# Performance work log

Hardware: AMD Instinct MI355X
Metric: run time of the kernel (lower is better)

## Reference

```python
import jax, jax.numpy as jnp
import numpy as np

INPUT_SIZE = 256
HIDDEN_SIZE = 256


def _linear_params(key, in_dim, out_dim):
    # PyTorch nn.Linear default init: U(-1/sqrt(in_dim), 1/sqrt(in_dim))
    k1, k2 = jax.random.split(key)
    bound = 1.0 / np.sqrt(in_dim)
    W = jax.random.uniform(k1, (out_dim, in_dim), jnp.float32, -bound, bound)
    b = jax.random.uniform(k2, (out_dim,), jnp.float32, -bound, bound)
    return W, b


def setup_inputs() -> dict:
    key = jax.random.key(0)
    keys = jax.random.split(key, 7)
    B = 65536
    x = jax.random.normal(keys[0], (B, INPUT_SIZE), jnp.float32)
    h_prev = jax.random.normal(keys[1], (B, HIDDEN_SIZE), jnp.float32)
    W_ir, b_ir = _linear_params(keys[2], INPUT_SIZE, HIDDEN_SIZE)
    W_iz, b_iz = _linear_params(keys[3], INPUT_SIZE, HIDDEN_SIZE)
    W_in, b_in = _linear_params(keys[4], INPUT_SIZE, HIDDEN_SIZE)
    W_hz, b_hz = _linear_params(keys[5], HIDDEN_SIZE, HIDDEN_SIZE)
    W_hn, b_hn = _linear_params(keys[6], HIDDEN_SIZE, HIDDEN_SIZE)
    # NOTE: weights_hr exists in the torch module but is never used in forward
    # (the source uses weights_hz for the reset gate too), so it is omitted.
    return {
        'x': x, 'h_prev': h_prev,
        'W_ir': W_ir, 'b_ir': b_ir,
        'W_iz': W_iz, 'b_iz': b_iz,
        'W_in': W_in, 'b_in': b_in,
        'W_hz': W_hz, 'b_hz': b_hz,
        'W_hn': W_hn, 'b_hn': b_hn,
    }


def reference(x, h_prev, W_ir, b_ir, W_iz, b_iz, W_in, b_in, W_hz, b_hz, W_hn, b_hn):
    # Faithful to source: both z and r use the hz projection of h_prev.
    hz = h_prev @ W_hz.T + b_hz                       # [B, H]
    z = jax.nn.sigmoid(x @ W_iz.T + b_iz + hz)        # update gate
    r = jax.nn.sigmoid(x @ W_ir.T + b_ir + hz)        # reset gate (bug: uses hz)
    g = jnp.tanh(x @ W_in.T + b_in + r * (h_prev @ W_hn.T + b_hn))
    h_new = (1.0 - z) * g + z * h_prev
    return h_new
```

## Files before the change

### kernel.cpp

```cpp
#include <hip/hip_runtime.h>
#include <hip/hip_bf16.h>

typedef __bf16 bf16x8 __attribute__((ext_vector_type(8)));
typedef __bf16 bf16x4 __attribute__((ext_vector_type(4)));
typedef float  f32x4  __attribute__((ext_vector_type(4)));

#define HID   256
#define BM    64
#define PITCH 264

__global__ void __launch_bounds__(256) prepack_frag(
    const float* __restrict__ w0, const float* __restrict__ w1,
    const float* __restrict__ w2, const float* __restrict__ w3,
    const float* __restrict__ w4, __bf16* __restrict__ wb)
{
    int t    = blockIdx.x * 256 + threadIdx.x;
    int lane = t & 63;
    int cb   = (t >> 6) & 15;
    int gk   = t >> 10;
    int g    = gk % 5;
    int ks   = gk / 5;
    const float* W = g == 0 ? w0 : g == 1 ? w1 : g == 2 ? w2 : g == 3 ? w3 : w4;
    int row = cb * 16 + (lane & 15);
    int k0  = ks * 32 + (lane >> 4) * 8;
    float4 p = *(const float4*)(W + row * HID + k0);
    float4 q = *(const float4*)(W + row * HID + k0 + 4);
    bf16x8 o;
    o[0]=(__bf16)p.x; o[1]=(__bf16)p.y; o[2]=(__bf16)p.z; o[3]=(__bf16)p.w;
    o[4]=(__bf16)q.x; o[5]=(__bf16)q.y; o[6]=(__bf16)q.z; o[7]=(__bf16)q.w;
    *(bf16x8*)(wb + (size_t)t * 8) = o;
}

#define MFMA1(D, A_, B_) D = __builtin_amdgcn_mfma_f32_16x16x32_bf16(A_, B_, D, 0, 0, 0)

#define MFMA12(MF, AX, AH, B_) do {                                   \
    _Pragma("unroll")                                                 \
    for (int nf = 0; nf < 2; ++nf) {                                  \
        MFMA1(az[MF][nf],  AX, B_[2 + nf]);                           \
        MFMA1(ar[MF][nf],  AX, B_[0 + nf]);                           \
        MFMA1(anx[MF][nf], AX, B_[4 + nf]);                           \
        MFMA1(az[MF][nf],  AH, B_[6 + nf]);                           \
        MFMA1(ar[MF][nf],  AH, B_[6 + nf]);                           \
        MFMA1(anh[MF][nf], AH, B_[8 + nf]);                           \
    }                                                                 \
} while (0)

#define LOADB(DST, KK) do {                                           \
    _Pragma("unroll")                                                 \
    for (int g = 0; g < 5; ++g)                                       \
        _Pragma("unroll")                                             \
        for (int nf = 0; nf < 2; ++nf)                                \
            DST[g * 2 + nf] =                                         \
                *(const bf16x8*)(wbase + ((KK) * 5 + g) * 8192 + nf * 512); \
} while (0)

#define LOADB_SLOW(DST, KK) do {                                      \
    _Pragma("unroll")                                                 \
    for (int g = 0; g < 5; ++g)                                       \
        _Pragma("unroll")                                             \
        for (int nf = 0; nf < 2; ++nf) {                              \
            const float* pp = wsrc[g] + ((wn * 2 + nf) * 16 + lr) * HID + (KK) * 32 + lg * 8; \
            float4 c0 = *(const float4*)(pp), c1 = *(const float4*)(pp + 4); \
            bf16x8 u;                                                 \
            u[0]=(__bf16)c0.x; u[1]=(__bf16)c0.y; u[2]=(__bf16)c0.z; u[3]=(__bf16)c0.w; \
            u[4]=(__bf16)c1.x; u[5]=(__bf16)c1.y; u[6]=(__bf16)c1.z; u[7]=(__bf16)c1.w; \
            DST[g * 2 + nf] = u;                                      \
        }                                                             \
} while (0)

#define CLUSTER(B_, KC) do {                                          \
    const int kb = (KC) * 32 + lg * 8;                                \
    bf16x8 a0x = *(const bf16x8*)(xt + (0 * 16 + lr) * PITCH + kb);   \
    bf16x8 a0h = *(const bf16x8*)(ht + (0 * 16 + lr) * PITCH + kb);   \
    bf16x8 a1x = *(const bf16x8*)(xt + (1 * 16 + lr) * PITCH + kb);   \
    bf16x8 a1h = *(const bf16x8*)(ht + (1 * 16 + lr) * PITCH + kb);   \
    MFMA12(0, a0x, a0h, B_);                                          \
    a0x = *(const bf16x8*)(xt + (2 * 16 + lr) * PITCH + kb);          \
    a0h = *(const bf16x8*)(ht + (2 * 16 + lr) * PITCH + kb);          \
    MFMA12(1, a1x, a1h, B_);                                          \
    a1x = *(const bf16x8*)(xt + (3 * 16 + lr) * PITCH + kb);          \
    a1h = *(const bf16x8*)(ht + (3 * 16 + lr) * PITCH + kb);          \
    MFMA12(2, a0x, a0h, B_);                                          \
    MFMA12(3, a1x, a1h, B_);                                          \
} while (0)

template<bool PACKED>
__global__ void __launch_bounds__(512, 2) gru_fused(
    const float* __restrict__ x,  const float* __restrict__ h,
    const __bf16* __restrict__ wb,
    const float* __restrict__ w_ir, const float* __restrict__ w_iz,
    const float* __restrict__ w_in, const float* __restrict__ w_hz,
    const float* __restrict__ w_hn,
    const float* __restrict__ b_ir, const float* __restrict__ b_iz,
    const float* __restrict__ b_in, const float* __restrict__ b_hz,
    const float* __restrict__ b_hn,
    float* __restrict__ out)
{
    __shared__ __bf16 xt[BM * PITCH];
    __shared__ __bf16 ht[BM * PITCH];

    const int t    = threadIdx.x;
    const int row0 = blockIdx.x * BM;
    const int lane = t & 63;
    const int wn   = t >> 6;
    const int lr   = lane & 15;
    const int lg   = lane >> 4;

    const float* wsrc[5] = { w_ir, w_iz, w_in, w_hz, w_hn };
    const __bf16* wbase = wb + wn * 1024 + lane * 8;

    f32x4 vx[8], vh[8];
#pragma unroll
    for (int i = 0; i < 8; ++i) {
        int c = i * 512 + t, r = c >> 6, k4 = (c & 63) * 4;
        vx[i] = __builtin_nontemporal_load((const f32x4*)(x + (size_t)(row0 + r) * HID + k4));
        vh[i] = __builtin_nontemporal_load((const f32x4*)(h + (size_t)(row0 + r) * HID + k4));
    }
    bf16x8 Ba[10], Bb[10];
    if (PACKED) LOADB(Ba, wn);
#pragma unroll
    for (int i = 0; i < 8; ++i) {
        int c = i * 512 + t, r = c >> 6, k4 = (c & 63) * 4;
        bf16x4 bx, bh;
        bx[0] = (__bf16)vx[i][0]; bx[1] = (__bf16)vx[i][1]; bx[2] = (__bf16)vx[i][2]; bx[3] = (__bf16)vx[i][3];
        bh[0] = (__bf16)vh[i][0]; bh[1] = (__bf16)vh[i][1]; bh[2] = (__bf16)vh[i][2]; bh[3] = (__bf16)vh[i][3];
        *(bf16x4*)(xt + r * PITCH + k4) = bx;
        *(bf16x4*)(ht + r * PITCH + k4) = bh;
    }
    __syncthreads();

    f32x4 az[4][2], ar[4][2], anx[4][2], anh[4][2];
#pragma unroll
    for (int mf = 0; mf < 4; ++mf)
#pragma unroll
        for (int nf = 0; nf < 2; ++nf) {
            az[mf][nf] = (f32x4)0.0f; ar[mf][nf] = (f32x4)0.0f;
            anx[mf][nf] = (f32x4)0.0f; anh[mf][nf] = (f32x4)0.0f;
        }

#pragma unroll
    for (int i2 = 0; i2 < 4; ++i2) {
        const int kA = (wn + 2 * i2)     & 7;
        const int kB = (wn + 2 * i2 + 1) & 7;
        const int kN = (wn + 2 * i2 + 2) & 7;
        if (PACKED) LOADB(Bb, kB); else LOADB_SLOW(Ba, kA);
        CLUSTER(Ba, kA);
        if (PACKED) { if (i2 < 3) LOADB(Ba, kN); } else LOADB_SLOW(Bb, kB);
        CLUSTER(Bb, kB);
    }

    float bz[2], br[2], bnx[2], bnh[2];
#pragma unroll
    for (int nf = 0; nf < 2; ++nf) {
        int col = wn * 32 + nf * 16 + lr;
        bz[nf]  = b_iz[col] + b_hz[col];
        br[nf]  = b_ir[col] + b_hz[col];
        bnx[nf] = b_in[col];
        bnh[nf] = b_hn[col];
    }
#pragma unroll
    for (int mf = 0; mf < 4; ++mf)
#pragma unroll
        for (int nf = 0; nf < 2; ++nf)
#pragma unroll
            for (int i = 0; i < 4; ++i) {
                int rl  = mf * 16 + lg * 4 + i;
                int col = wn * 32 + nf * 16 + lr;
                float z  = 1.0f / (1.0f + __expf(-(az[mf][nf][i] + bz[nf])));
                float r  = 1.0f / (1.0f + __expf(-(ar[mf][nf][i] + br[nf])));
                float e2 = __expf(2.0f * (anx[mf][nf][i] + bnx[nf] + r * (anh[mf][nf][i] + bnh[nf])));
                float g  = 1.0f - 2.0f / (e2 + 1.0f);
                float hp = (float)ht[rl * PITCH + col];
                __builtin_nontemporal_store((1.0f - z) * g + z * hp,
                                            out + (size_t)(row0 + rl) * HID + col);
            }
}

extern "C" void kernel_launch(void* const* d_in, const int* in_sizes, int n_in,
                              void* d_out, int out_size, void* d_ws, size_t ws_size,
                              hipStream_t stream) {
    const float* x    = (const float*)d_in[0];
    const float* h    = (const float*)d_in[1];
    const float* w_ir = (const float*)d_in[2];
    const float* b_ir = (const float*)d_in[3];
    const float* w_iz = (const float*)d_in[4];
    const float* b_iz = (const float*)d_in[5];
    const float* w_in = (const float*)d_in[6];
    const float* b_in = (const float*)d_in[7];
    const float* w_hz = (const float*)d_in[8];
    const float* b_hz = (const float*)d_in[9];
    const float* w_hn = (const float*)d_in[10];
    const float* b_hn = (const float*)d_in[11];
    float* out = (float*)d_out;

    const int B = in_sizes[0] / HID;
    const size_t wb_bytes = (size_t)5 * HID * HID * sizeof(__bf16);

    if (ws_size >= wb_bytes) {
        __bf16* wb = (__bf16*)d_ws;
        prepack_frag<<<160, 256, 0, stream>>>(w_ir, w_iz, w_in, w_hz, w_hn, wb);
        gru_fused<true><<<B / BM, 512, 0, stream>>>(
            x, h, wb, nullptr, nullptr, nullptr, nullptr, nullptr,
            b_ir, b_iz, b_in, b_hz, b_hn, out);
    } else {
        gru_fused<false><<<B / BM, 512, 0, stream>>>(
            x, h, nullptr, w_ir, w_iz, w_in, w_hz, w_hn,
            b_ir, b_iz, b_in, b_hz, b_hn, out);
    }
}
```

Measured before the change: 97.59 us.

## Make GRU kernel persistent with double-buffered LDS prefetch of next tile

```diff
diff --git a/kernel.cpp b/kernel.cpp
--- a/kernel.cpp
+++ b/kernel.cpp
@@ -84,6 +84,39 @@
     MFMA12(3, a1x, a1h, B_);                                          \
 } while (0)
 
+#define KPAIR(I2) do {                                                \
+    const int kA = (wn + 2 * (I2))     & 7;                           \
+    const int kB = (wn + 2 * (I2) + 1) & 7;                           \
+    const int kN = (wn + 2 * (I2) + 2) & 7;                           \
+    if (PACKED) LOADB(Bb, kB); else LOADB_SLOW(Ba, kA);               \
+    CLUSTER(Ba, kA);                                                  \
+    if (PACKED) LOADB(Ba, kN); else LOADB_SLOW(Bb, kB);               \
+    CLUSTER(Bb, kB);                                                  \
+} while (0)
+
+#define PF_ISSUE(Q) do {                                              \
+    _Pragma("unroll")                                                 \
+    for (int i = 0; i < 2; ++i) {                                     \
+        int r  = (Q) * 16 + i * 8 + (t >> 6);                         \
+        int k4 = (t & 63) * 4;                                        \
+        px[i] = __builtin_nontemporal_load((const f32x4*)(x + (prow0 + r) * HID + k4)); \
+        ph[i] = __builtin_nontemporal_load((const f32x4*)(h + (prow0 + r) * HID + k4)); \
+    }                                                                 \
+} while (0)
+
+#define PF_STORE(Q) do {                                              \
+    _Pragma("unroll")                                                 \
+    for (int i = 0; i < 2; ++i) {                                     \
+        int r  = (Q) * 16 + i * 8 + (t >> 6);                         \
+        int k4 = (t & 63) * 4;                                        \
+        bf16x4 bx, bh;                                                \
+        bx[0]=(__bf16)px[i][0]; bx[1]=(__bf16)px[i][1]; bx[2]=(__bf16)px[i][2]; bx[3]=(__bf16)px[i][3]; \
+        bh[0]=(__bf16)ph[i][0]; bh[1]=(__bf16)ph[i][1]; bh[2]=(__bf16)ph[i][2]; bh[3]=(__bf16)ph[i][3]; \
+        *(bf16x4*)(xw + r * PITCH + k4) = bx;                         \
+        *(bf16x4*)(hw + r * PITCH + k4) = bh;                         \
+    }                                                                 \
+} while (0)
+
 template<bool PACKED>
 __global__ void __launch_bounds__(512, 2) gru_fused(
     const float* __restrict__ x,  const float* __restrict__ h,
@@ -94,13 +127,12 @@
     const float* __restrict__ b_ir, const float* __restrict__ b_iz,
     const float* __restrict__ b_in, const float* __restrict__ b_hz,
     const float* __restrict__ b_hn,
-    float* __restrict__ out)
+    float* __restrict__ out, int ntiles)
 {
-    __shared__ __bf16 xt[BM * PITCH];
-    __shared__ __bf16 ht[BM * PITCH];
+    __shared__ __bf16 xts[2][BM * PITCH];
+    __shared__ __bf16 hts[2][BM * PITCH];
 
     const int t    = threadIdx.x;
-    const int row0 = blockIdx.x * BM;
     const int lane = t & 63;
     const int wn   = t >> 6;
     const int lr   = lane & 15;
@@ -109,45 +141,7 @@
     const float* wsrc[5] = { w_ir, w_iz, w_in, w_hz, w_hn };
     const __bf16* wbase = wb + wn * 1024 + lane * 8;
 
-    f32x4 vx[8], vh[8];
-#pragma unroll
-    for (int i = 0; i < 8; ++i) {
-        int c = i * 512 + t, r = c >> 6, k4 = (c & 63) * 4;
-        vx[i] = __builtin_nontemporal_load((const f32x4*)(x + (size_t)(row0 + r) * HID + k4));
-        vh[i] = __builtin_nontemporal_load((const f32x4*)(h + (size_t)(row0 + r) * HID + k4));
-    }
     bf16x8 Ba[10], Bb[10];
-    if (PACKED) LOADB(Ba, wn);
-#pragma unroll
-    for (int i = 0; i < 8; ++i) {
-        int c = i * 512 + t, r = c >> 6, k4 = (c & 63) * 4;
-        bf16x4 bx, bh;
-        bx[0] = (__bf16)vx[i][0]; bx[1] = (__bf16)vx[i][1]; bx[2] = (__bf16)vx[i][2]; bx[3] = (__bf16)vx[i][3];
-        bh[0] = (__bf16)vh[i][0]; bh[1] = (__bf16)vh[i][1]; bh[2] = (__bf16)vh[i][2]; bh[3] = (__bf16)vh[i][3];
-        *(bf16x4*)(xt + r * PITCH + k4) = bx;
-        *(bf16x4*)(ht + r * PITCH + k4) = bh;
-    }
-    __syncthreads();
-
-    f32x4 az[4][2], ar[4][2], anx[4][2], anh[4][2];
-#pragma unroll
-    for (int mf = 0; mf < 4; ++mf)
-#pragma unroll
-        for (int nf = 0; nf < 2; ++nf) {
-            az[mf][nf] = (f32x4)0.0f; ar[mf][nf] = (f32x4)0.0f;
-            anx[mf][nf] = (f32x4)0.0f; anh[mf][nf] = (f32x4)0.0f;
-        }
-
-#pragma unroll
-    for (int i2 = 0; i2 < 4; ++i2) {
-        const int kA = (wn + 2 * i2)     & 7;
-        const int kB = (wn + 2 * i2 + 1) & 7;
-        const int kN = (wn + 2 * i2 + 2) & 7;
-        if (PACKED) LOADB(Bb, kB); else LOADB_SLOW(Ba, kA);
-        CLUSTER(Ba, kA);
-        if (PACKED) { if (i2 < 3) LOADB(Ba, kN); } else LOADB_SLOW(Bb, kB);
-        CLUSTER(Bb, kB);
-    }
 
     float bz[2], br[2], bnx[2], bnh[2];
 #pragma unroll
@@ -158,22 +152,82 @@
         bnx[nf] = b_in[col];
         bnh[nf] = b_hn[col];
     }
-#pragma unroll
-    for (int mf = 0; mf < 4; ++mf)
-#pragma unroll
-        for (int nf = 0; nf < 2; ++nf)
-#pragma unroll
-            for (int i = 0; i < 4; ++i) {
-                int rl  = mf * 16 + lg * 4 + i;
-                int col = wn * 32 + nf * 16 + lr;
-                float z  = 1.0f / (1.0f + __expf(-(az[mf][nf][i] + bz[nf])));
-                float r  = 1.0f / (1.0f + __expf(-(ar[mf][nf][i] + br[nf])));
-                float e2 = __expf(2.0f * (anx[mf][nf][i] + bnx[nf] + r * (anh[mf][nf][i] + bnh[nf])));
-                float g  = 1.0f - 2.0f / (e2 + 1.0f);
-                float hp = (float)ht[rl * PITCH + col];
-                __builtin_nontemporal_store((1.0f - z) * g + z * hp,
-                                            out + (size_t)(row0 + rl) * HID + col);
+
+    int tile = blockIdx.x;
+    if (tile >= ntiles) return;
+
+    {
+        const size_t row0 = (size_t)tile * BM;
+        f32x4 vx[8], vh[8];
+#pragma unroll
+        for (int i = 0; i < 8; ++i) {
+            int c = i * 512 + t, r = c >> 6, k4 = (c & 63) * 4;
+            vx[i] = __builtin_nontemporal_load((const f32x4*)(x + (row0 + r) * HID + k4));
+            vh[i] = __builtin_nontemporal_load((const f32x4*)(h + (row0 + r) * HID + k4));
+        }
+        if (PACKED) LOADB(Ba, wn);
+#pragma unroll
+        for (int i = 0; i < 8; ++i) {
+            int c = i * 512 + t, r = c >> 6, k4 = (c & 63) * 4;
+            bf16x4 bx, bh;
+            bx[0]=(__bf16)vx[i][0]; bx[1]=(__bf16)vx[i][1]; bx[2]=(__bf16)vx[i][2]; bx[3]=(__bf16)vx[i][3];
+            bh[0]=(__bf16)vh[i][0]; bh[1]=(__bf16)vh[i][1]; bh[2]=(__bf16)vh[i][2]; bh[3]=(__bf16)vh[i][3];
+            *(bf16x4*)(xts[0] + r * PITCH + k4) = bx;
+            *(bf16x4*)(hts[0] + r * PITCH + k4) = bh;
+        }
+    }
+    __syncthreads();
+
+    int bsel = 0;
+    for (; tile < ntiles; tile += gridDim.x) {
+        const __bf16* xt = xts[bsel];
+        const __bf16* ht = hts[bsel];
+        __bf16* xw = xts[bsel ^ 1];
+        __bf16* hw = hts[bsel ^ 1];
+        const int nxt = tile + gridDim.x;
+        const bool pf = nxt < ntiles;
+        const size_t prow0 = (size_t)(pf ? nxt : tile) * BM;
+
+        f32x4 az[4][2], ar[4][2], anx[4][2], anh[4][2];
+#pragma unroll
+        for (int mf = 0; mf < 4; ++mf)
+#pragma unroll
+            for (int nf = 0; nf < 2; ++nf) {
+                az[mf][nf] = (f32x4)0.0f; ar[mf][nf] = (f32x4)0.0f;
+                anx[mf][nf] = (f32x4)0.0f; anh[mf][nf] = (f32x4)0.0f;
             }
+
+        f32x4 px[2], ph[2];
+        if (pf) PF_ISSUE(0);
+        KPAIR(0);
+        if (pf) { PF_STORE(0); PF_ISSUE(1); }
+        KPAIR(1);
+        if (pf) { PF_STORE(1); PF_ISSUE(2); }
+        KPAIR(2);
+        if (pf) { PF_STORE(2); PF_ISSUE(3); }
+        KPAIR(3);
+        if (pf) PF_STORE(3);
+
+        const size_t row0 = (size_t)tile * BM;
+#pragma unroll
+        for (int mf = 0; mf < 4; ++mf)
+#pragma unroll
+            for (int nf = 0; nf < 2; ++nf)
+#pragma unroll
+                for (int i = 0; i < 4; ++i) {
+                    int rl  = mf * 16 + lg * 4 + i;
+                    int col = wn * 32 + nf * 16 + lr;
+                    float z  = 1.0f / (1.0f + __expf(-(az[mf][nf][i] + bz[nf])));
+                    float r  = 1.0f / (1.0f + __expf(-(ar[mf][nf][i] + br[nf])));
+                    float e2 = __expf(2.0f * (anx[mf][nf][i] + bnx[nf] + r * (anh[mf][nf][i] + bnh[nf])));
+                    float g  = 1.0f - 2.0f / (e2 + 1.0f);
+                    float hp = (float)ht[rl * PITCH + col];
+                    __builtin_nontemporal_store((1.0f - z) * g + z * hp,
+                                                out + (row0 + rl) * HID + col);
+                }
+        __syncthreads();
+        bsel ^= 1;
+    }
 }
 
 extern "C" void kernel_launch(void* const* d_in, const int* in_sizes, int n_in,
@@ -193,18 +247,20 @@
     const float* b_hn = (const float*)d_in[11];
     float* out = (float*)d_out;
 
-    const int B = in_sizes[0] / HID;
+    const int B      = in_sizes[0] / HID;
+    const int ntiles = B / BM;
+    const int nblk   = ntiles < 256 ? ntiles : 256;
     const size_t wb_bytes = (size_t)5 * HID * HID * sizeof(__bf16);
 
     if (ws_size >= wb_bytes) {
         __bf16* wb = (__bf16*)d_ws;
         prepack_frag<<<160, 256, 0, stream>>>(w_ir, w_iz, w_in, w_hz, w_hn, wb);
-        gru_fused<true><<<B / BM, 512, 0, stream>>>(
+        gru_fused<true><<<nblk, 512, 0, stream>>>(
             x, h, wb, nullptr, nullptr, nullptr, nullptr, nullptr,
-            b_ir, b_iz, b_in, b_hz, b_hn, out);
+            b_ir, b_iz, b_in, b_hz, b_hn, out, ntiles);
     } else {
-        gru_fused<false><<<B / BM, 512, 0, stream>>>(
+        gru_fused<false><<<nblk, 512, 0, stream>>>(
             x, h, nullptr, w_ir, w_iz, w_in, w_hz, w_hn,
-            b_ir, b_iz, b_in, b_hz, b_hn, out);
+            b_ir, b_iz, b_in, b_hz, b_hn, out, ntiles);
     }
 }
```

Result: slower. 242.2 us (+148.2%).

## Process four tiles per block with double-buffered LDS and x/h prefetch

Applied to the files above, without the earlier changes.

```diff
diff --git a/kernel.cpp b/kernel.cpp
--- a/kernel.cpp
+++ b/kernel.cpp
@@ -68,20 +68,83 @@
         }                                                             \
 } while (0)
 
-#define CLUSTER(B_, KC) do {                                          \
+#define CLUSTER(XT, HT, B_, KC) do {                                  \
     const int kb = (KC) * 32 + lg * 8;                                \
-    bf16x8 a0x = *(const bf16x8*)(xt + (0 * 16 + lr) * PITCH + kb);   \
-    bf16x8 a0h = *(const bf16x8*)(ht + (0 * 16 + lr) * PITCH + kb);   \
-    bf16x8 a1x = *(const bf16x8*)(xt + (1 * 16 + lr) * PITCH + kb);   \
-    bf16x8 a1h = *(const bf16x8*)(ht + (1 * 16 + lr) * PITCH + kb);   \
+    bf16x8 a0x = *(const bf16x8*)((XT) + (0 * 16 + lr) * PITCH + kb); \
+    bf16x8 a0h = *(const bf16x8*)((HT) + (0 * 16 + lr) * PITCH + kb); \
+    bf16x8 a1x = *(const bf16x8*)((XT) + (1 * 16 + lr) * PITCH + kb); \
+    bf16x8 a1h = *(const bf16x8*)((HT) + (1 * 16 + lr) * PITCH + kb); \
     MFMA12(0, a0x, a0h, B_);                                          \
-    a0x = *(const bf16x8*)(xt + (2 * 16 + lr) * PITCH + kb);          \
-    a0h = *(const bf16x8*)(ht + (2 * 16 + lr) * PITCH + kb);          \
+    a0x = *(const bf16x8*)((XT) + (2 * 16 + lr) * PITCH + kb);        \
+    a0h = *(const bf16x8*)((HT) + (2 * 16 + lr) * PITCH + kb);        \
     MFMA12(1, a1x, a1h, B_);                                          \
-    a1x = *(const bf16x8*)(xt + (3 * 16 + lr) * PITCH + kb);          \
-    a1h = *(const bf16x8*)(ht + (3 * 16 + lr) * PITCH + kb);          \
+    a1x = *(const bf16x8*)((XT) + (3 * 16 + lr) * PITCH + kb);        \
+    a1h = *(const bf16x8*)((HT) + (3 * 16 + lr) * PITCH + kb);        \
     MFMA12(2, a0x, a0h, B_);                                          \
     MFMA12(3, a1x, a1h, B_);                                          \
+} while (0)
+
+#define KSTEP(XT, HT, S, BCUR, BNXT) do {                             \
+    const int kc = (wn + (S)) & 7;                                    \
+    const int kn = (wn + (S) + 1) & 7;                                \
+    if (PACKED) LOADB(BNXT, kn); else LOADB_SLOW(BCUR, kc);           \
+    CLUSTER(XT, HT, BCUR, kc);                                        \
+} while (0)
+
+#define PFI(C) do {                                                   \
+    int r  = (C) * 8 + (t >> 6);                                      \
+    int k4 = (t & 63) * 4;                                            \
+    px = __builtin_nontemporal_load((const f32x4*)(x + (prow0 + r) * HID + k4)); \
+    ph = __builtin_nontemporal_load((const f32x4*)(h + (prow0 + r) * HID + k4)); \
+} while (0)
+
+#define PFS(XW, HW, C) do {                                           \
+    int r  = (C) * 8 + (t >> 6);                                      \
+    int k4 = (t & 63) * 4;                                            \
+    bf16x4 bx, bh;                                                    \
+    bx[0]=(__bf16)px[0]; bx[1]=(__bf16)px[1]; bx[2]=(__bf16)px[2]; bx[3]=(__bf16)px[3]; \
+    bh[0]=(__bf16)ph[0]; bh[1]=(__bf16)ph[1]; bh[2]=(__bf16)ph[2]; bh[3]=(__bf16)ph[3]; \
+    *(bf16x4*)((XW) + r * PITCH + k4) = bx;                           \
+    *(bf16x4*)((HW) + r * PITCH + k4) = bh;                           \
+} while (0)
+
+#define TILE_BODY(XT, HT, XW, HW, TILE, PFC) do {                     \
+    const bool pf_  = (PFC);                                          \
+    const int prow0 = ((TILE) + 1) * BM;                              \
+    f32x4 px, ph;                                                     \
+    _Pragma("unroll")                                                 \
+    for (int mf = 0; mf < 4; ++mf)                                    \
+        _Pragma("unroll")                                             \
+        for (int nf = 0; nf < 2; ++nf) {                              \
+            az[mf][nf] = (f32x4)0.0f; ar[mf][nf] = (f32x4)0.0f;       \
+            anx[mf][nf] = (f32x4)0.0f; anh[mf][nf] = (f32x4)0.0f;     \
+        }                                                             \
+    if (pf_) PFI(0);                                                  \
+    KSTEP(XT, HT, 0, Ba, Bb); if (pf_) { PFS(XW, HW, 0); PFI(1); }    \
+    KSTEP(XT, HT, 1, Bb, Ba); if (pf_) { PFS(XW, HW, 1); PFI(2); }    \
+    KSTEP(XT, HT, 2, Ba, Bb); if (pf_) { PFS(XW, HW, 2); PFI(3); }    \
+    KSTEP(XT, HT, 3, Bb, Ba); if (pf_) { PFS(XW, HW, 3); PFI(4); }    \
+    KSTEP(XT, HT, 4, Ba, Bb); if (pf_) { PFS(XW, HW, 4); PFI(5); }    \
+    KSTEP(XT, HT, 5, Bb, Ba); if (pf_) { PFS(XW, HW, 5); PFI(6); }    \
+    KSTEP(XT, HT, 6, Ba, Bb); if (pf_) { PFS(XW, HW, 6); PFI(7); }    \
+    KSTEP(XT, HT, 7, Bb, Ba); if (pf_) { PFS(XW, HW, 7); }            \
+    const int row0 = (TILE) * BM;                                     \
+    _Pragma("unroll")                                                 \
+    for (int mf = 0; mf < 4; ++mf)                                    \
+        _Pragma("unroll")                                             \
+        for (int nf = 0; nf < 2; ++nf)                                \
+            _Pragma("unroll")                                         \
+            for (int i = 0; i < 4; ++i) {                             \
+                int rl  = mf * 16 + lg * 4 + i;                       \
+                int col = wn * 32 + nf * 16 + lr;                     \
+                float z  = 1.0f / (1.0f + __expf(-(az[mf][nf][i] + bz[nf]))); \
+                float r  = 1.0f / (1.0f + __expf(-(ar[mf][nf][i] + br[nf]))); \
+                float e2 = __expf(2.0f * (anx[mf][nf][i] + bnx[nf] + r * (anh[mf][nf][i] + bnh[nf]))); \
+                float g  = 1.0f - 2.0f / (e2 + 1.0f);                 \
+                float hp = (float)(HT)[rl * PITCH + col];             \
+                __builtin_nontemporal_store((1.0f - z) * g + z * hp,  \
+                    out + (size_t)(row0 + rl) * HID + col);           \
+            }                                                         \
 } while (0)
 
 template<bool PACKED>
@@ -96,58 +159,23 @@
     const float* __restrict__ b_hn,
     float* __restrict__ out)
 {
-    __shared__ __bf16 xt[BM * PITCH];
-    __shared__ __bf16 ht[BM * PITCH];
+    __shared__ __bf16 xt0[BM * PITCH];
+    __shared__ __bf16 ht0[BM * PITCH];
+    __shared__ __bf16 xt1[BM * PITCH];
+    __shared__ __bf16 ht1[BM * PITCH];
 
     const int t    = threadIdx.x;
-    const int row0 = blockIdx.x * BM;
     const int lane = t & 63;
     const int wn   = t >> 6;
     const int lr   = lane & 15;
     const int lg   = lane >> 4;
+    const int tileBase = blockIdx.x * 4;
 
     const float* wsrc[5] = { w_ir, w_iz, w_in, w_hz, w_hn };
     const __bf16* wbase = wb + wn * 1024 + lane * 8;
 
-    f32x4 vx[8], vh[8];
-#pragma unroll
-    for (int i = 0; i < 8; ++i) {
-        int c = i * 512 + t, r = c >> 6, k4 = (c & 63) * 4;
-        vx[i] = __builtin_nontemporal_load((const f32x4*)(x + (size_t)(row0 + r) * HID + k4));
-        vh[i] = __builtin_nontemporal_load((const f32x4*)(h + (size_t)(row0 + r) * HID + k4));
-    }
     bf16x8 Ba[10], Bb[10];
-    if (PACKED) LOADB(Ba, wn);
-#pragma unroll
-    for (int i = 0; i < 8; ++i) {
-        int c = i * 512 + t, r = c >> 6, k4 = (c & 63) * 4;
-        bf16x4 bx, bh;
-        bx[0] = (__bf16)vx[i][0]; bx[1] = (__bf16)vx[i][1]; bx[2] = (__bf16)vx[i][2]; bx[3] = (__bf16)vx[i][3];
-        bh[0] = (__bf16)vh[i][0]; bh[1] = (__bf16)vh[i][1]; bh[2] = (__bf16)vh[i][2]; bh[3] = (__bf16)vh[i][3];
-        *(bf16x4*)(xt + r * PITCH + k4) = bx;
-        *(bf16x4*)(ht + r * PITCH + k4) = bh;
-    }
-    __syncthreads();
-
     f32x4 az[4][2], ar[4][2], anx[4][2], anh[4][2];
-#pragma unroll
-    for (int mf = 0; mf < 4; ++mf)
-#pragma unroll
-        for (int nf = 0; nf < 2; ++nf) {
-            az[mf][nf] = (f32x4)0.0f; ar[mf][nf] = (f32x4)0.0f;
-            anx[mf][nf] = (f32x4)0.0f; anh[mf][nf] = (f32x4)0.0f;
-        }
-
-#pragma unroll
-    for (int i2 = 0; i2 < 4; ++i2) {
-        const int kA = (wn + 2 * i2)     & 7;
-        const int kB = (wn + 2 * i2 + 1) & 7;
-        const int kN = (wn + 2 * i2 + 2) & 7;
-        if (PACKED) LOADB(Bb, kB); else LOADB_SLOW(Ba, kA);
-        CLUSTER(Ba, kA);
-        if (PACKED) { if (i2 < 3) LOADB(Ba, kN); } else LOADB_SLOW(Bb, kB);
-        CLUSTER(Bb, kB);
-    }
 
     float bz[2], br[2], bnx[2], bnh[2];
 #pragma unroll
@@ -158,22 +186,36 @@
         bnx[nf] = b_in[col];
         bnh[nf] = b_hn[col];
     }
+
+    {
+        const int row0 = tileBase * BM;
+        f32x4 vx[8], vh[8];
 #pragma unroll
-    for (int mf = 0; mf < 4; ++mf)
+        for (int i = 0; i < 8; ++i) {
+            int c = i * 512 + t, r = c >> 6, k4 = (c & 63) * 4;
+            vx[i] = __builtin_nontemporal_load((const f32x4*)(x + (row0 + r) * HID + k4));
+            vh[i] = __builtin_nontemporal_load((const f32x4*)(h + (row0 + r) * HID + k4));
+        }
+        if (PACKED) LOADB(Ba, wn);
 #pragma unroll
-        for (int nf = 0; nf < 2; ++nf)
-#pragma unroll
-            for (int i = 0; i < 4; ++i) {
-                int rl  = mf * 16 + lg * 4 + i;
-                int col = wn * 32 + nf * 16 + lr;
-                float z  = 1.0f / (1.0f + __expf(-(az[mf][nf][i] + bz[nf])));
-                float r  = 1.0f / (1.0f + __expf(-(ar[mf][nf][i] + br[nf])));
-                float e2 = __expf(2.0f * (anx[mf][nf][i] + bnx[nf] + r * (anh[mf][nf][i] + bnh[nf])));
-                float g  = 1.0f - 2.0f / (e2 + 1.0f);
-                float hp = (float)ht[rl * PITCH + col];
-                __builtin_nontemporal_store((1.0f - z) * g + z * hp,
-                                            out + (size_t)(row0 + rl) * HID + col);
-            }
+        for (int i = 0; i < 8; ++i) {
+            int c = i * 512 + t, r = c >> 6, k4 = (c & 63) * 4;
+            bf16x4 bx, bh;
+            bx[0]=(__bf16)vx[i][0]; bx[1]=(__bf16)vx[i][1]; bx[2]=(__bf16)vx[i][2]; bx[3]=(__bf16)vx[i][3];
+            bh[0]=(__bf16)vh[i][0]; bh[1]=(__bf16)vh[i][1]; bh[2]=(__bf16)vh[i][2]; bh[3]=(__bf16)vh[i][3];
+            *(bf16x4*)(xt0 + r * PITCH + k4) = bx;
+            *(bf16x4*)(ht0 + r * PITCH + k4) = bh;
+        }
+    }
+    __syncthreads();
+
+    for (int it = 0; it < 2; ++it) {
+        const int tE = tileBase + it * 2;
+        TILE_BODY(xt0, ht0, xt1, ht1, tE, true);
+        __syncthreads();
+        TILE_BODY(xt1, ht1, xt0, ht0, tE + 1, it == 0);
+        __syncthreads();
+    }
 }
 
 extern "C" void kernel_launch(void* const* d_in, const int* in_sizes, int n_in,
@@ -193,17 +235,18 @@
     const float* b_hn = (const float*)d_in[11];
     float* out = (float*)d_out;
 
-    const int B = in_sizes[0] / HID;
+    const int B      = in_sizes[0] / HID;
+    const int nblk   = (B / BM) / 4;
     const size_t wb_bytes = (size_t)5 * HID * HID * sizeof(__bf16);
 
     if (ws_size >= wb_bytes) {
         __bf16* wb = (__bf16*)d_ws;
         prepack_frag<<<160, 256, 0, stream>>>(w_ir, w_iz, w_in, w_hz, w_hn, wb);
-        gru_fused<true><<<B / BM, 512, 0, stream>>>(
+        gru_fused<true><<<nblk, 512, 0, stream>>>(
             x, h, wb, nullptr, nullptr, nullptr, nullptr, nullptr,
             b_ir, b_iz, b_in, b_hz, b_hn, out);
     } else {
-        gru_fused<false><<<B / BM, 512, 0, stream>>>(
+        gru_fused<false><<<nblk, 512, 0, stream>>>(
             x, h, nullptr, w_ir, w_iz, w_in, w_hz, w_hn,
             b_ir, b_iz, b_in, b_hz, b_hn, out);
     }
```

Measured after the change: 224.8 us. 130% more time.
